# Kernel tuning notes

Measured on AMD Instinct MI355X. Metric: run time of the kernel, lower is better.

## Reference

```python
import jax, jax.numpy as jnp
import numpy as np

HIDDEN = 256
DEPTH = 3
MOL_ATOMS = 42  # padding_final_size in MPNEncoder.padding (AM_dim0=False)
ATOM_FDIM = 133
BOND_FDIM = 147
N_MOLS = 4000
N_ATOMS = N_MOLS * MOL_ATOMS
N_BONDS = 360000
MAX_NB = 6


def setup_inputs() -> dict:
    key = jax.random.key(0)
    ks = jax.random.split(key, 9)
    f_atoms = jax.random.normal(ks[0], (N_ATOMS, ATOM_FDIM), dtype=jnp.float32)
    f_bonds = jax.random.normal(ks[1], (N_BONDS, BOND_FDIM), dtype=jnp.float32)
    a2b = jax.random.randint(ks[2], (N_ATOMS, MAX_NB), 0, N_BONDS, dtype=jnp.int32)
    b2a = jax.random.randint(ks[3], (N_BONDS,), 0, N_ATOMS, dtype=jnp.int32)
    b2revb = jax.random.randint(ks[4], (N_BONDS,), 0, N_BONDS, dtype=jnp.int32)
    # learned params (bias=False for W_i/W_h, W_o has bias, per chemprop defaults)
    W_i = jax.random.normal(ks[5], (HIDDEN, BOND_FDIM), dtype=jnp.float32) * 0.05
    W_h = jax.random.normal(ks[6], (HIDDEN, HIDDEN), dtype=jnp.float32) * 0.05
    W_o = jax.random.normal(ks[7], (HIDDEN, ATOM_FDIM + HIDDEN), dtype=jnp.float32) * 0.05
    b_o = jax.random.normal(ks[8], (HIDDEN,), dtype=jnp.float32) * 0.05
    return dict(f_atoms=f_atoms, f_bonds=f_bonds, W_i=W_i, W_h=W_h, W_o=W_o,
                b_o=b_o, a2b=a2b, b2a=b2a, b2revb=b2revb)


def reference(f_atoms, f_bonds, W_i, W_h, W_o, b_o, a2b, b2a, b2revb):
    # bond-message MPN (atom_messages=False, undirected=False, dropout=0)
    relu = jax.nn.relu
    inp = f_bonds @ W_i.T                         # [n_bonds, H]
    message = relu(inp)

    def atom_hidden(a_msg):
        a_input = jnp.concatenate([f_atoms, a_msg], axis=1)  # [n_atoms, fa+H]
        return relu(a_input @ W_o.T + b_o)

    # depth-0 hidden: a_input = [f_atoms, zeros(H)] (the 'padding' tensor)
    save_depth = [atom_hidden(jnp.zeros((f_atoms.shape[0], HIDDEN), f_atoms.dtype))]
    for d in range(DEPTH - 1):
        if d == 0:
            save_depth.append(atom_hidden(message[a2b].sum(axis=1)))
        a_message = message[a2b].sum(axis=1)      # gather+sum over neighbors
        message = a_message[b2a] - message[b2revb]
        message = relu(inp + message @ W_h.T)
        save_depth.append(atom_hidden(message[a2b].sum(axis=1)))

    # every molecule has exactly MOL_ATOMS atoms -> padding() is identity,
    # per-molecule narrow/stack becomes a reshape
    def pool(h):
        return h.reshape(N_MOLS, MOL_ATOMS, HIDDEN)

    d0, d1, d2 = pool(save_depth[0]), pool(save_depth[1]), pool(save_depth[2])
    dfin = pool(save_depth[-1])
    mol_vecs = dfin.mean(axis=1)                  # sum / a_size
    return (d0, d1, d2, dfin, mol_vecs)
```

## Files before the change

kernel.cpp:

```cpp
#include <hip/hip_runtime.h>

typedef unsigned short u16;
typedef unsigned int u32;
typedef __bf16 bf16x8 __attribute__((ext_vector_type(8)));
typedef float f32x4 __attribute__((ext_vector_type(4)));

__device__ __forceinline__ float bf2f(u16 h) {
  union { u32 u; float f; } c; c.u = ((u32)h) << 16; return c.f;
}
__device__ __forceinline__ float bflo(u32 u) {
  union { u32 u; float f; } c; c.u = u << 16; return c.f;
}
__device__ __forceinline__ float bfhi(u32 u) {
  union { u32 u; float f; } c; c.u = u & 0xffff0000u; return c.f;
}
__device__ __forceinline__ u32 pack2bf(float a, float b) {
  union { __bf16 h[2]; u32 u; } c; c.h[0] = (__bf16)a; c.h[1] = (__bf16)b;
  return c.u;
}
__device__ __forceinline__ u16 f2bf(float f) {
  union { __bf16 h; u16 u; } c; c.h = (__bf16)f; return c.u;
}
__device__ __forceinline__ float relu(float x) { return x > 0.f ? x : 0.f; }

__global__ __launch_bounds__(256) void cvt_w(const float* __restrict__ src,
                                             u16* __restrict__ dst, int N,
                                             int Ks, int Kd, int src_stride,
                                             int col0) {
  int i = blockIdx.x * 256 + threadIdx.x;
  if (i >= N * Kd) return;
  int n = i / Kd, k = i % Kd;
  float v = (k < Ks) ? src[(size_t)n * src_stride + col0 + k] : 0.f;
  dst[i] = f2bf(v);
}

template <int ASRC, int EPI, int KPAD>
__global__ __launch_bounds__(256, 3) void gemm5(
    const float* __restrict__ Af, int Kreal,
    const u16* __restrict__ Ab, const u16* __restrict__ Ab2,
    const int* __restrict__ idx1, const int* __restrict__ idx2,
    const u16* __restrict__ Bw,
    const u16* __restrict__ addb, const float* __restrict__ bias,
    u16* __restrict__ outb0, float* __restrict__ outf) {
  constexpr int LDK = KPAD + 8;
  __shared__ u16 As[64 * LDK];

  const int tid = threadIdx.x;
  const int lane = tid & 63;
  const int wn = (tid >> 6) * 64;
  const int m0 = blockIdx.x * 64;
  const int lm = lane & 15, lg = lane >> 4;
  const int koff = lg * 8;

  if constexpr (ASRC == 0) {
#pragma unroll
    for (int p = 0; p < 64 * KPAD / 512; ++p) {
      int e = (p * 256 + tid) * 2;
      int row = e / KPAD, k = e % KPAD;
      const float* src = Af + (size_t)(m0 + row) * Kreal + k;
      float x0 = (k < Kreal) ? src[0] : 0.f;
      float x1 = (k + 1 < Kreal) ? src[1] : 0.f;
      *reinterpret_cast<u32*>(&As[row * LDK + k]) = pack2bf(x0, x1);
    }
  } else if constexpr (ASRC == 1) {
#pragma unroll
    for (int p = 0; p < 64 * KPAD / 8 / 256; ++p) {
      int ch = p * 256 + tid;
      int row = ch / (KPAD / 8), c8 = ch % (KPAD / 8);
      uint4 v = *reinterpret_cast<const uint4*>(Ab + (size_t)(m0 + row) * KPAD + c8 * 8);
      *reinterpret_cast<uint4*>(&As[row * LDK + c8 * 8]) = v;
    }
  } else {
    static_assert(KPAD == 256, "ASRC2 assumes KPAD=256");
    const int row = tid >> 2, seg = tid & 3;
    const int gr = m0 + row;
    const int r1 = idx1[gr], r2 = idx2[gr];
    const u16* pa = Ab + (size_t)r1 * KPAD + seg * 64;
    const u16* pb = Ab2 + (size_t)r2 * KPAD + seg * 64;
    uint4 va[8], vb[8];
#pragma unroll
    for (int i = 0; i < 8; ++i) va[i] = *reinterpret_cast<const uint4*>(pa + i * 8);
#pragma unroll
    for (int i = 0; i < 8; ++i) vb[i] = *reinterpret_cast<const uint4*>(pb + i * 8);
    u16* dst = &As[row * LDK + seg * 64];
#pragma unroll
    for (int i = 0; i < 8; ++i) {
      uint4 o;
      o.x = pack2bf(bflo(va[i].x) - relu(bflo(vb[i].x)),
                    bfhi(va[i].x) - relu(bfhi(vb[i].x)));
      o.y = pack2bf(bflo(va[i].y) - relu(bflo(vb[i].y)),
                    bfhi(va[i].y) - relu(bfhi(vb[i].y)));
      o.z = pack2bf(bflo(va[i].z) - relu(bflo(vb[i].z)),
                    bfhi(va[i].z) - relu(bfhi(vb[i].z)));
      o.w = pack2bf(bflo(va[i].w) - relu(bflo(vb[i].w)),
                    bfhi(va[i].w) - relu(bfhi(vb[i].w)));
      *reinterpret_cast<uint4*>(dst + i * 8) = o;
    }
  }
  __syncthreads();

  f32x4 acc[4][4];
#pragma unroll
  for (int i = 0; i < 4; ++i)
#pragma unroll
    for (int j = 0; j < 4; ++j) acc[i][j] = (f32x4)(0.f);

#pragma unroll
  for (int kk = 0; kk < KPAD / 32; ++kk) {
    const int k0 = kk * 32 + koff;
    bf16x8 a[4];
#pragma unroll
    for (int im = 0; im < 4; ++im)
      a[im] = *reinterpret_cast<const bf16x8*>(&As[(im * 16 + lm) * LDK + k0]);
#pragma unroll
    for (int jw = 0; jw < 4; ++jw) {
      bf16x8 b = *reinterpret_cast<const bf16x8*>(
          Bw + (size_t)(wn + jw * 16 + lm) * KPAD + k0);
#pragma unroll
      for (int im = 0; im < 4; ++im)
        acc[im][jw] = __builtin_amdgcn_mfma_f32_16x16x32_bf16(b, a[im], acc[im][jw], 0, 0, 0);
    }
  }

#pragma unroll
  for (int im = 0; im < 4; ++im) {
#pragma unroll
    for (int jw = 0; jw < 4; ++jw) {
      const int r = m0 + im * 16 + lm;
      const int c0 = wn + jw * 16 + lg * 4;
      const size_t idx = (size_t)r * 256 + c0;
      f32x4 v = acc[im][jw];
      if constexpr (EPI == 0) {
        uint2 o; o.x = pack2bf(v[0], v[1]); o.y = pack2bf(v[2], v[3]);
        *reinterpret_cast<uint2*>(outb0 + idx) = o;
      } else if constexpr (EPI == 1) {
        const float4 bb = *reinterpret_cast<const float4*>(bias + c0);
        v[0] += bb.x; v[1] += bb.y; v[2] += bb.z; v[3] += bb.w;
        uint2 o; o.x = pack2bf(v[0], v[1]); o.y = pack2bf(v[2], v[3]);
        *reinterpret_cast<uint2*>(outb0 + idx) = o;
        float4 rl = {relu(v[0]), relu(v[1]), relu(v[2]), relu(v[3])};
        *reinterpret_cast<float4*>(outf + idx) = rl;
      } else if constexpr (EPI == 2) {
        const uint2 ab = *reinterpret_cast<const uint2*>(addb + idx);
        v[0] += bflo(ab.x); v[1] += bfhi(ab.x);
        v[2] += bflo(ab.y); v[3] += bfhi(ab.y);
        uint2 o; o.x = pack2bf(v[0], v[1]); o.y = pack2bf(v[2], v[3]);
        *reinterpret_cast<uint2*>(outb0 + idx) = o;
      } else {
        const uint2 ab = *reinterpret_cast<const uint2*>(addb + idx);
        v[0] += bflo(ab.x); v[1] += bfhi(ab.x);
        v[2] += bflo(ab.y); v[3] += bfhi(ab.y);
        float4 rl = {relu(v[0]), relu(v[1]), relu(v[2]), relu(v[3])};
        *reinterpret_cast<float4*>(outf + idx) = rl;
      }
    }
  }
}

__global__ __launch_bounds__(256) void gather_sum(const u16* __restrict__ S,
                                                  const int* __restrict__ a2b,
                                                  u16* __restrict__ amsg,
                                                  int n_atoms) {
  int wave = threadIdx.x >> 6, lane = threadIdx.x & 63;
  int atom = blockIdx.x * 4 + wave;
  if (atom >= n_atoms) return;
  float s0 = 0.f, s1 = 0.f, s2 = 0.f, s3 = 0.f;
  int base = atom * 6;
#pragma unroll
  for (int j = 0; j < 6; ++j) {
    int b = a2b[base + j];
    ushort4 v = *reinterpret_cast<const ushort4*>(S + (size_t)b * 256 + lane * 4);
    s0 += relu(bf2f(v.x));
    s1 += relu(bf2f(v.y));
    s2 += relu(bf2f(v.z));
    s3 += relu(bf2f(v.w));
  }
  uint2 o;
  o.x = pack2bf(s0, s1);
  o.y = pack2bf(s2, s3);
  *reinterpret_cast<uint2*>(amsg + (size_t)atom * 256 + lane * 4) = o;
}

__global__ __launch_bounds__(256) void mol_mean(const float* __restrict__ dfin,
                                                float* __restrict__ out) {
  int mol = blockIdx.x, c = threadIdx.x;
  const float* p = dfin + (size_t)mol * (42 * 256) + c;
  float s = 0.f;
#pragma unroll
  for (int a = 0; a < 42; ++a) s += p[a * 256];
  out[(size_t)mol * 256 + c] = s * (1.0f / 42.0f);
}

extern "C" void kernel_launch(void* const* d_in, const int* in_sizes, int n_in,
                              void* d_out, int out_size, void* d_ws,
                              size_t ws_size, hipStream_t stream) {
  const float* f_atoms = (const float*)d_in[0];
  const float* f_bonds = (const float*)d_in[1];
  const float* W_i = (const float*)d_in[2];
  const float* W_h = (const float*)d_in[3];
  const float* W_o = (const float*)d_in[4];
  const float* b_o = (const float*)d_in[5];
  const int* a2b = (const int*)d_in[6];
  const int* b2a = (const int*)d_in[7];
  const int* b2revb = (const int*)d_in[8];

  const int NA = 168000, NB = 360000, H = 256;
  const size_t SZ_BH = (size_t)NB * H * 2;
  const size_t SZ_AH = (size_t)NA * H * 2;

  char* ws = (char*)d_ws;
  u16* inp_b = (u16*)ws;  ws += SZ_BH;
  u16* P0    = (u16*)ws;  ws += SZ_BH;
  u16* P1    = (u16*)ws;  ws += SZ_BH;
  u16* amsg  = (u16*)ws;  ws += SZ_AH;
  u16* base_b = (u16*)ws; ws += SZ_AH;
  u16* Wi_b  = (u16*)ws;  ws += 256 * 160 * 2;
  u16* Wh_b  = (u16*)ws;  ws += 256 * 256 * 2;
  u16* Wo1_b = (u16*)ws;  ws += 256 * 160 * 2;
  u16* Wo2_b = (u16*)ws;  ws += 256 * 256 * 2;

  float* out = (float*)d_out;
  float* d0 = out;
  float* d1 = d0 + (size_t)NA * H;
  float* d2 = d1 + (size_t)NA * H;
  float* dfin = d2 + (size_t)NA * H;
  float* mol = dfin + (size_t)NA * H;

  dim3 blk(256);
  cvt_w<<<dim3((256 * 160 + 255) / 256), blk, 0, stream>>>(W_i, Wi_b, 256, 147, 160, 147, 0);
  cvt_w<<<dim3((256 * 256 + 255) / 256), blk, 0, stream>>>(W_h, Wh_b, 256, 256, 256, 256, 0);
  cvt_w<<<dim3((256 * 160 + 255) / 256), blk, 0, stream>>>(W_o, Wo1_b, 256, 133, 160, 389, 0);
  cvt_w<<<dim3((256 * 256 + 255) / 256), blk, 0, stream>>>(W_o, Wo2_b, 256, 256, 256, 389, 133);

  gemm5<0, 0, 160><<<dim3(NB / 64), blk, 0, stream>>>(
      f_bonds, 147, nullptr, nullptr, nullptr, nullptr, Wi_b,
      nullptr, nullptr, inp_b, nullptr);
  gemm5<0, 1, 160><<<dim3(NA / 64), blk, 0, stream>>>(
      f_atoms, 133, nullptr, nullptr, nullptr, nullptr, Wo1_b,
      nullptr, b_o, base_b, d0);

  u16* S = inp_b;
  u16* pms[2] = {P0, P1};
  float* douts[3] = {d1, d2, dfin};
  for (int d = 0; d < 3; ++d) {
    gather_sum<<<dim3(NA / 4), blk, 0, stream>>>(S, a2b, amsg, NA);
    gemm5<1, 3, 256><<<dim3(NA / 64), blk, 0, stream>>>(
        nullptr, 0, amsg, nullptr, nullptr, nullptr, Wo2_b,
        base_b, nullptr, nullptr, douts[d]);
    if (d < 2) {
      gemm5<2, 2, 256><<<dim3(NB / 64), blk, 0, stream>>>(
          nullptr, 0, amsg, S, b2a, b2revb, Wh_b,
          inp_b, nullptr, pms[d], nullptr);
      S = pms[d];
    }
  }
  mol_mean<<<dim3(4000), blk, 0, stream>>>(dfin, mol);
}
```

Measured before the change: 1.553 ms.

## Use async global-to-LDS loads with swizzled layout and split Wh GEMM by linearity

Input features are pre-converted to padded bf16 buffers so the GEMMs can fill LDS with direct global_load_lds 16-byte copies into an XOR-swizzled layout instead of converting through registers. The message recurrence now stores post-ReLU messages, which drops the ReLU from the gather. The Wh GEMM computes amsg[b2a]·W and M[b2revb]·W as two separate MFMA accumulations and subtracts them in the epilogue rather than forming the difference in LDS. The four weight-conversion launches are merged into one and occupancy is raised to 4 blocks. In exchange the change adds extra conversion passes and workspace, doubles the MFMA work in the Wh GEMM, and slightly changes bf16 rounding.

Result: slower. 1.664 ms (+7.1%).

```diff
diff --git a/kernel.cpp b/kernel.cpp
--- a/kernel.cpp
+++ b/kernel.cpp
@@ -23,79 +23,67 @@
 }
 __device__ __forceinline__ float relu(float x) { return x > 0.f ? x : 0.f; }
 
-__global__ __launch_bounds__(256) void cvt_w(const float* __restrict__ src,
-                                             u16* __restrict__ dst, int N,
-                                             int Ks, int Kd, int src_stride,
-                                             int col0) {
+typedef __attribute__((address_space(1))) const u32* gas_t;
+typedef __attribute__((address_space(3))) u32* las_t;
+__device__ __forceinline__ void async16(const void* g, void* l) {
+  __builtin_amdgcn_global_load_lds((gas_t)g, (las_t)l, 16, 0, 0);
+}
+
+__global__ __launch_bounds__(256) void cvt_all(
+    const float* __restrict__ Wi, const float* __restrict__ Wh,
+    const float* __restrict__ Wo, u16* __restrict__ dWi, u16* __restrict__ dWh,
+    u16* __restrict__ dWo1, u16* __restrict__ dWo2) {
   int i = blockIdx.x * 256 + threadIdx.x;
-  if (i >= N * Kd) return;
-  int n = i / Kd, k = i % Kd;
-  float v = (k < Ks) ? src[(size_t)n * src_stride + col0 + k] : 0.f;
-  dst[i] = f2bf(v);
-}
-
-template <int ASRC, int EPI, int KPAD>
-__global__ __launch_bounds__(256, 3) void gemm5(
-    const float* __restrict__ Af, int Kreal,
-    const u16* __restrict__ Ab, const u16* __restrict__ Ab2,
-    const int* __restrict__ idx1, const int* __restrict__ idx2,
-    const u16* __restrict__ Bw,
+  if (i < 40960) {
+    int n = i / 160, k = i % 160;
+    dWi[i] = f2bf(k < 147 ? Wi[n * 147 + k] : 0.f);
+  } else if (i < 106496) {
+    int j = i - 40960;
+    dWh[j] = f2bf(Wh[j]);
+  } else if (i < 147456) {
+    int j = i - 106496;
+    int n = j / 160, k = j % 160;
+    dWo1[j] = f2bf(k < 133 ? Wo[n * 389 + k] : 0.f);
+  } else {
+    int j = i - 147456;
+    int n = j / 256, k = j % 256;
+    dWo2[j] = f2bf(Wo[n * 389 + 133 + k]);
+  }
+}
+
+__global__ __launch_bounds__(256) void cvt_feat(const float* __restrict__ src,
+                                                u16* __restrict__ dst,
+                                                int Ks, int Kd, long total) {
+  long i = (long)blockIdx.x * 256 + threadIdx.x;
+  if (i >= total) return;
+  int row = (int)(i / Kd), k = (int)(i % Kd);
+  dst[i] = f2bf(k < Ks ? src[(size_t)row * Ks + k] : 0.f);
+}
+
+template <int KPAD, int EPI>
+__global__ __launch_bounds__(256, 4) void gemm_async(
+    const u16* __restrict__ Ab, const u16* __restrict__ Bw,
     const u16* __restrict__ addb, const float* __restrict__ bias,
-    u16* __restrict__ outb0, float* __restrict__ outf) {
-  constexpr int LDK = KPAD + 8;
-  __shared__ u16 As[64 * LDK];
+    u16* __restrict__ outb0, u16* __restrict__ outb1,
+    float* __restrict__ outf) {
+  constexpr int CPR = KPAD / 8;
+  constexpr int XM = (KPAD == 256) ? 7 : 3;
+  constexpr int IPW = CPR / 4;
+  __shared__ u16 As[64 * KPAD];
 
   const int tid = threadIdx.x;
-  const int lane = tid & 63;
-  const int wn = (tid >> 6) * 64;
+  const int lane = tid & 63, wid = tid >> 6;
+  const int wn = wid * 64;
   const int m0 = blockIdx.x * 64;
   const int lm = lane & 15, lg = lane >> 4;
-  const int koff = lg * 8;
-
-  if constexpr (ASRC == 0) {
-#pragma unroll
-    for (int p = 0; p < 64 * KPAD / 512; ++p) {
-      int e = (p * 256 + tid) * 2;
-      int row = e / KPAD, k = e % KPAD;
-      const float* src = Af + (size_t)(m0 + row) * Kreal + k;
-      float x0 = (k < Kreal) ? src[0] : 0.f;
-      float x1 = (k + 1 < Kreal) ? src[1] : 0.f;
-      *reinterpret_cast<u32*>(&As[row * LDK + k]) = pack2bf(x0, x1);
-    }
-  } else if constexpr (ASRC == 1) {
-#pragma unroll
-    for (int p = 0; p < 64 * KPAD / 8 / 256; ++p) {
-      int ch = p * 256 + tid;
-      int row = ch / (KPAD / 8), c8 = ch % (KPAD / 8);
-      uint4 v = *reinterpret_cast<const uint4*>(Ab + (size_t)(m0 + row) * KPAD + c8 * 8);
-      *reinterpret_cast<uint4*>(&As[row * LDK + c8 * 8]) = v;
-    }
-  } else {
-    static_assert(KPAD == 256, "ASRC2 assumes KPAD=256");
-    const int row = tid >> 2, seg = tid & 3;
-    const int gr = m0 + row;
-    const int r1 = idx1[gr], r2 = idx2[gr];
-    const u16* pa = Ab + (size_t)r1 * KPAD + seg * 64;
-    const u16* pb = Ab2 + (size_t)r2 * KPAD + seg * 64;
-    uint4 va[8], vb[8];
-#pragma unroll
-    for (int i = 0; i < 8; ++i) va[i] = *reinterpret_cast<const uint4*>(pa + i * 8);
-#pragma unroll
-    for (int i = 0; i < 8; ++i) vb[i] = *reinterpret_cast<const uint4*>(pb + i * 8);
-    u16* dst = &As[row * LDK + seg * 64];
-#pragma unroll
-    for (int i = 0; i < 8; ++i) {
-      uint4 o;
-      o.x = pack2bf(bflo(va[i].x) - relu(bflo(vb[i].x)),
-                    bfhi(va[i].x) - relu(bfhi(vb[i].x)));
-      o.y = pack2bf(bflo(va[i].y) - relu(bflo(vb[i].y)),
-                    bfhi(va[i].y) - relu(bfhi(vb[i].y)));
-      o.z = pack2bf(bflo(va[i].z) - relu(bflo(vb[i].z)),
-                    bfhi(va[i].z) - relu(bfhi(vb[i].z)));
-      o.w = pack2bf(bflo(va[i].w) - relu(bflo(vb[i].w)),
-                    bfhi(va[i].w) - relu(bfhi(vb[i].w)));
-      *reinterpret_cast<uint4*>(dst + i * 8) = o;
-    }
+
+#pragma unroll
+  for (int p = 0; p < IPW; ++p) {
+    const int q = wid * IPW + p;
+    const int chunk = q * 64 + lane;
+    const int row = chunk / CPR, k8 = chunk % CPR;
+    const u16* src = Ab + (size_t)(m0 + row) * KPAD + (k8 ^ (row & XM)) * 8;
+    async16(src, &As[q * 512]);
   }
   __syncthreads();
 
@@ -107,18 +95,20 @@
 
 #pragma unroll
   for (int kk = 0; kk < KPAD / 32; ++kk) {
-    const int k0 = kk * 32 + koff;
     bf16x8 a[4];
 #pragma unroll
-    for (int im = 0; im < 4; ++im)
-      a[im] = *reinterpret_cast<const bf16x8*>(&As[(im * 16 + lm) * LDK + k0]);
+    for (int t = 0; t < 4; ++t) {
+      const int row = t * 16 + lm;
+      const int phys = (kk * 4 + lg) ^ (row & XM);
+      a[t] = *reinterpret_cast<const bf16x8*>(&As[row * KPAD + phys * 8]);
+    }
 #pragma unroll
     for (int jw = 0; jw < 4; ++jw) {
       bf16x8 b = *reinterpret_cast<const bf16x8*>(
-          Bw + (size_t)(wn + jw * 16 + lm) * KPAD + k0);
-#pragma unroll
-      for (int im = 0; im < 4; ++im)
-        acc[im][jw] = __builtin_amdgcn_mfma_f32_16x16x32_bf16(b, a[im], acc[im][jw], 0, 0, 0);
+          Bw + (size_t)(wn + jw * 16 + lm) * KPAD + kk * 32 + lg * 8);
+#pragma unroll
+      for (int t = 0; t < 4; ++t)
+        acc[t][jw] = __builtin_amdgcn_mfma_f32_16x16x32_bf16(b, a[t], acc[t][jw], 0, 0, 0);
     }
   }
 
@@ -133,6 +123,9 @@
       if constexpr (EPI == 0) {
         uint2 o; o.x = pack2bf(v[0], v[1]); o.y = pack2bf(v[2], v[3]);
         *reinterpret_cast<uint2*>(outb0 + idx) = o;
+        uint2 m; m.x = pack2bf(relu(v[0]), relu(v[1]));
+        m.y = pack2bf(relu(v[2]), relu(v[3]));
+        *reinterpret_cast<uint2*>(outb1 + idx) = m;
       } else if constexpr (EPI == 1) {
         const float4 bb = *reinterpret_cast<const float4*>(bias + c0);
         v[0] += bb.x; v[1] += bb.y; v[2] += bb.z; v[3] += bb.w;
@@ -140,12 +133,6 @@
         *reinterpret_cast<uint2*>(outb0 + idx) = o;
         float4 rl = {relu(v[0]), relu(v[1]), relu(v[2]), relu(v[3])};
         *reinterpret_cast<float4*>(outf + idx) = rl;
-      } else if constexpr (EPI == 2) {
-        const uint2 ab = *reinterpret_cast<const uint2*>(addb + idx);
-        v[0] += bflo(ab.x); v[1] += bfhi(ab.x);
-        v[2] += bflo(ab.y); v[3] += bfhi(ab.y);
-        uint2 o; o.x = pack2bf(v[0], v[1]); o.y = pack2bf(v[2], v[3]);
-        *reinterpret_cast<uint2*>(outb0 + idx) = o;
       } else {
         const uint2 ab = *reinterpret_cast<const uint2*>(addb + idx);
         v[0] += bflo(ab.x); v[1] += bfhi(ab.x);
@@ -157,7 +144,78 @@
   }
 }
 
-__global__ __launch_bounds__(256) void gather_sum(const u16* __restrict__ S,
+__global__ __launch_bounds__(256, 4) void gemm_wh(
+    const u16* __restrict__ amsg, const u16* __restrict__ M,
+    const int* __restrict__ b2a, const int* __restrict__ b2revb,
+    const u16* __restrict__ Bw, const u16* __restrict__ inp,
+    u16* __restrict__ outM) {
+  __shared__ u16 Aa[32 * 256];
+  __shared__ u16 Am[32 * 256];
+
+  const int tid = threadIdx.x;
+  const int lane = tid & 63, wid = tid >> 6;
+  const int wn = wid * 64;
+  const int m0 = blockIdx.x * 32;
+  const int lm = lane & 15, lg = lane >> 4;
+
+#pragma unroll
+  for (int p = 0; p < 4; ++p) {
+    const int q = wid * 4 + p;
+    const int chunk = q * 64 + lane;
+    const int row = chunk >> 5, k8 = chunk & 31;
+    const int soff = (k8 ^ (row & 7)) * 8;
+    const int r1 = b2a[m0 + row];
+    async16(amsg + (size_t)r1 * 256 + soff, &Aa[q * 512]);
+    const int r2 = b2revb[m0 + row];
+    async16(M + (size_t)r2 * 256 + soff, &Am[q * 512]);
+  }
+  __syncthreads();
+
+  f32x4 ac1[2][4], ac2[2][4];
+#pragma unroll
+  for (int i = 0; i < 2; ++i)
+#pragma unroll
+    for (int j = 0; j < 4; ++j) { ac1[i][j] = (f32x4)(0.f); ac2[i][j] = (f32x4)(0.f); }
+
+#pragma unroll
+  for (int kk = 0; kk < 8; ++kk) {
+    const int phys = (kk * 4 + lg) ^ (lm & 7);
+    bf16x8 aa0 = *reinterpret_cast<const bf16x8*>(&Aa[lm * 256 + phys * 8]);
+    bf16x8 aa1 = *reinterpret_cast<const bf16x8*>(&Aa[(16 + lm) * 256 + phys * 8]);
+    bf16x8 am0 = *reinterpret_cast<const bf16x8*>(&Am[lm * 256 + phys * 8]);
+    bf16x8 am1 = *reinterpret_cast<const bf16x8*>(&Am[(16 + lm) * 256 + phys * 8]);
+#pragma unroll
+    for (int jw = 0; jw < 4; ++jw) {
+      bf16x8 b = *reinterpret_cast<const bf16x8*>(
+          Bw + (size_t)(wn + jw * 16 + lm) * 256 + kk * 32 + lg * 8);
+      ac1[0][jw] = __builtin_amdgcn_mfma_f32_16x16x32_bf16(b, aa0, ac1[0][jw], 0, 0, 0);
+      ac1[1][jw] = __builtin_amdgcn_mfma_f32_16x16x32_bf16(b, aa1, ac1[1][jw], 0, 0, 0);
+      ac2[0][jw] = __builtin_amdgcn_mfma_f32_16x16x32_bf16(b, am0, ac2[0][jw], 0, 0, 0);
+      ac2[1][jw] = __builtin_amdgcn_mfma_f32_16x16x32_bf16(b, am1, ac2[1][jw], 0, 0, 0);
+    }
+  }
+
+#pragma unroll
+  for (int im = 0; im < 2; ++im) {
+#pragma unroll
+    for (int jw = 0; jw < 4; ++jw) {
+      const int r = m0 + im * 16 + lm;
+      const int c0 = wn + jw * 16 + lg * 4;
+      const size_t idx = (size_t)r * 256 + c0;
+      const uint2 ab = *reinterpret_cast<const uint2*>(inp + idx);
+      float v0 = ac1[im][jw][0] - ac2[im][jw][0] + bflo(ab.x);
+      float v1 = ac1[im][jw][1] - ac2[im][jw][1] + bfhi(ab.x);
+      float v2 = ac1[im][jw][2] - ac2[im][jw][2] + bflo(ab.y);
+      float v3 = ac1[im][jw][3] - ac2[im][jw][3] + bfhi(ab.y);
+      uint2 o;
+      o.x = pack2bf(relu(v0), relu(v1));
+      o.y = pack2bf(relu(v2), relu(v3));
+      *reinterpret_cast<uint2*>(outM + idx) = o;
+    }
+  }
+}
+
+__global__ __launch_bounds__(256) void gather_sum(const u16* __restrict__ M,
                                                   const int* __restrict__ a2b,
                                                   u16* __restrict__ amsg,
                                                   int n_atoms) {
@@ -169,11 +227,9 @@
 #pragma unroll
   for (int j = 0; j < 6; ++j) {
     int b = a2b[base + j];
-    ushort4 v = *reinterpret_cast<const ushort4*>(S + (size_t)b * 256 + lane * 4);
-    s0 += relu(bf2f(v.x));
-    s1 += relu(bf2f(v.y));
-    s2 += relu(bf2f(v.z));
-    s3 += relu(bf2f(v.w));
+    uint2 v = *reinterpret_cast<const uint2*>(M + (size_t)b * 256 + lane * 4);
+    s0 += bflo(v.x); s1 += bfhi(v.x);
+    s2 += bflo(v.y); s3 += bfhi(v.y);
   }
   uint2 o;
   o.x = pack2bf(s0, s1);
@@ -209,9 +265,12 @@
   const size_t SZ_AH = (size_t)NA * H * 2;
 
   char* ws = (char*)d_ws;
+  u16* fb16  = (u16*)ws;  ws += (size_t)NB * 160 * 2;
+  u16* fa16  = (u16*)ws;  ws += (size_t)NA * 160 * 2;
   u16* inp_b = (u16*)ws;  ws += SZ_BH;
-  u16* P0    = (u16*)ws;  ws += SZ_BH;
-  u16* P1    = (u16*)ws;  ws += SZ_BH;
+  u16* M0    = (u16*)ws;  ws += SZ_BH;
+  u16* M1    = (u16*)ws;  ws += SZ_BH;
+  u16* M2    = (u16*)ws;  ws += SZ_BH;
   u16* amsg  = (u16*)ws;  ws += SZ_AH;
   u16* base_b = (u16*)ws; ws += SZ_AH;
   u16* Wi_b  = (u16*)ws;  ws += 256 * 160 * 2;
@@ -227,31 +286,26 @@
   float* mol = dfin + (size_t)NA * H;
 
   dim3 blk(256);
-  cvt_w<<<dim3((256 * 160 + 255) / 256), blk, 0, stream>>>(W_i, Wi_b, 256, 147, 160, 147, 0);
-  cvt_w<<<dim3((256 * 256 + 255) / 256), blk, 0, stream>>>(W_h, Wh_b, 256, 256, 256, 256, 0);
-  cvt_w<<<dim3((256 * 160 + 255) / 256), blk, 0, stream>>>(W_o, Wo1_b, 256, 133, 160, 389, 0);
-  cvt_w<<<dim3((256 * 256 + 255) / 256), blk, 0, stream>>>(W_o, Wo2_b, 256, 256, 256, 389, 133);
-
-  gemm5<0, 0, 160><<<dim3(NB / 64), blk, 0, stream>>>(
-      f_bonds, 147, nullptr, nullptr, nullptr, nullptr, Wi_b,
-      nullptr, nullptr, inp_b, nullptr);
-  gemm5<0, 1, 160><<<dim3(NA / 64), blk, 0, stream>>>(
-      f_atoms, 133, nullptr, nullptr, nullptr, nullptr, Wo1_b,
-      nullptr, b_o, base_b, d0);
-
-  u16* S = inp_b;
-  u16* pms[2] = {P0, P1};
+  cvt_all<<<dim3(832), blk, 0, stream>>>(W_i, W_h, W_o, Wi_b, Wh_b, Wo1_b, Wo2_b);
+  cvt_feat<<<dim3((int)(((long)NB * 160 + 255) / 256)), blk, 0, stream>>>(
+      f_bonds, fb16, 147, 160, (long)NB * 160);
+  cvt_feat<<<dim3((int)(((long)NA * 160 + 255) / 256)), blk, 0, stream>>>(
+      f_atoms, fa16, 133, 160, (long)NA * 160);
+
+  gemm_async<160, 0><<<dim3(NB / 64), blk, 0, stream>>>(
+      fb16, Wi_b, nullptr, nullptr, inp_b, M0, nullptr);
+  gemm_async<160, 1><<<dim3(NA / 64), blk, 0, stream>>>(
+      fa16, Wo1_b, nullptr, b_o, base_b, nullptr, d0);
+
+  u16* Ms[3] = {M0, M1, M2};
   float* douts[3] = {d1, d2, dfin};
   for (int d = 0; d < 3; ++d) {
-    gather_sum<<<dim3(NA / 4), blk, 0, stream>>>(S, a2b, amsg, NA);
-    gemm5<1, 3, 256><<<dim3(NA / 64), blk, 0, stream>>>(
-        nullptr, 0, amsg, nullptr, nullptr, nullptr, Wo2_b,
-        base_b, nullptr, nullptr, douts[d]);
+    gather_sum<<<dim3(NA / 4), blk, 0, stream>>>(Ms[d], a2b, amsg, NA);
+    gemm_async<256, 3><<<dim3(NA / 64), blk, 0, stream>>>(
+        amsg, Wo2_b, base_b, nullptr, nullptr, nullptr, douts[d]);
     if (d < 2) {
-      gemm5<2, 2, 256><<<dim3(NB / 64), blk, 0, stream>>>(
-          nullptr, 0, amsg, S, b2a, b2revb, Wh_b,
-          inp_b, nullptr, pms[d], nullptr);
-      S = pms[d];
+      gemm_wh<<<dim3(NB / 32), blk, 0, stream>>>(
+          amsg, Ms[d], b2a, b2revb, Wh_b, inp_b, Ms[d + 1]);
     }
   }
   mol_mean<<<dim3(4000), blk, 0, stream>>>(dfin, mol);
```
